# Kernel tuning notes

Hardware: AMD Instinct MI355X
Metric: run time of the kernel (lower is better)

The kernel has to match this reference:

```python
import jax, jax.numpy as jnp
import numpy as np

D_MODEL = 1024
N_HEADS = 16
D_FF = 512  # FeedForward default d_ff=512 (not overridden in EncoderLayer)
EPS = 1e-6


def _norm(x, alpha, bias):
    # Custom NormLayer: mean + UNBIASED variance (torch.var default, N-1 denom)
    mean = jnp.mean(x, axis=-1, keepdims=True)
    n = x.shape[-1]
    var = jnp.sum((x - mean) ** 2, axis=-1, keepdims=True) / (n - 1)
    return alpha * (x - mean) / jnp.sqrt(var + EPS) + bias


def setup_inputs() -> dict:
    key = jax.random.key(0)
    ks = jax.random.split(key, 12)
    s = 1.0 / np.sqrt(D_MODEL)
    inp = {
        "x": jax.random.normal(ks[0], (2, 2048, D_MODEL), dtype=jnp.float32),
        "Wq": jax.random.uniform(ks[1], (D_MODEL, D_MODEL), jnp.float32, -s, s),
        "bq": jnp.zeros((D_MODEL,), jnp.float32),
        "Wk": jax.random.uniform(ks[2], (D_MODEL, D_MODEL), jnp.float32, -s, s),
        "bk": jnp.zeros((D_MODEL,), jnp.float32),
        "Wv": jax.random.uniform(ks[3], (D_MODEL, D_MODEL), jnp.float32, -s, s),
        "bv": jnp.zeros((D_MODEL,), jnp.float32),
        "Wo": jax.random.uniform(ks[4], (D_MODEL, D_MODEL), jnp.float32, -s, s),
        "bo": jnp.zeros((D_MODEL,), jnp.float32),
        "alpha1": jnp.ones((D_MODEL,), jnp.float32),
        "beta1": jnp.zeros((D_MODEL,), jnp.float32),
        "alpha2": jnp.ones((D_MODEL,), jnp.float32),
        "beta2": jnp.zeros((D_MODEL,), jnp.float32),
        "W1": jax.random.uniform(ks[5], (D_MODEL, D_FF), jnp.float32, -s, s),
        "b1": jnp.zeros((D_FF,), jnp.float32),
        "W2": jax.random.uniform(ks[6], (D_FF, D_MODEL), jnp.float32, -1.0 / np.sqrt(D_FF), 1.0 / np.sqrt(D_FF)),
        "b2": jnp.zeros((D_MODEL,), jnp.float32),
    }
    return inp


def reference(x, Wq, bq, Wk, bk, Wv, bv, Wo, bo, alpha1, beta1, alpha2, beta2, W1, b1, W2, b2):
    B, S, D = x.shape
    H = N_HEADS
    dh = D // H
    # norm_1 applied to x, result feeds BOTH attention and the residual
    x = _norm(x, alpha1, beta1)
    # multihead attention (dropout = identity in eval)
    q = (x @ Wq + bq).reshape(B, S, H, dh)
    k = (x @ Wk + bk).reshape(B, S, H, dh)
    v = (x @ Wv + bv).reshape(B, S, H, dh)
    scores = jnp.einsum("bqhd,bkhd->bhqk", q, k) / jnp.sqrt(jnp.asarray(dh, x.dtype))
    attn = jax.nn.softmax(scores, axis=-1)
    o = jnp.einsum("bhqk,bkhd->bqhd", attn, v).reshape(B, S, D)
    o = o @ Wo + bo
    x = x + o
    # FFN on norm_2(x)
    h = _norm(x, alpha2, beta2)
    h = jax.nn.relu(h @ W1 + b1) @ W2 + b2
    return x + h
```

## Files before the change

kernel.cpp:

```cpp
#include <hip/hip_runtime.h>

typedef __bf16 bf16;
typedef __bf16 bf16x4 __attribute__((ext_vector_type(4)));
typedef __bf16 bf16x8 __attribute__((ext_vector_type(8)));
typedef float f32x4 __attribute__((ext_vector_type(4)));

#define D_MODEL 1024
#define SEQ 2048
#define NB 2
#define LOG2E 1.4426950408889634f

__device__ __forceinline__ void glds16(const bf16* g, bf16* l) {
    __builtin_amdgcn_global_load_lds(
        (const __attribute__((address_space(1))) void*)g,
        (__attribute__((address_space(3))) void*)l, 16, 0, 0);
}

__device__ __forceinline__ void tile_tcvt(
    const float* __restrict__ src, int rows, int cols, bf16* __restrict__ dst,
    int bx, int by, bf16 (*t)[72])
{
    int tid = threadIdx.x;
    int k0 = by * 64, n0 = bx * 64;
    int r = tid >> 2, c = (tid & 3) * 16;
    const float4* s = (const float4*)(src + (size_t)(k0 + r) * cols + n0 + c);
#pragma unroll
    for (int q = 0; q < 4; ++q) {
        float4 v = s[q];
        t[c + q * 4 + 0][r] = (bf16)v.x;
        t[c + q * 4 + 1][r] = (bf16)v.y;
        t[c + q * 4 + 2][r] = (bf16)v.z;
        t[c + q * 4 + 3][r] = (bf16)v.w;
    }
    __syncthreads();
    bf16* d = dst + (size_t)(n0 + r) * rows + k0 + c;
    *(bf16x8*)(d)     = *(const bf16x8*)&t[r][c];
    *(bf16x8*)(d + 8) = *(const bf16x8*)&t[r][c + 8];
}

__global__ __launch_bounds__(256) void prep_kernel(
    const float* __restrict__ Wq, const float* __restrict__ Wk,
    const float* __restrict__ Wv, const float* __restrict__ Wo,
    const float* __restrict__ W1, const float* __restrict__ W2,
    const float* __restrict__ bq, const float* __restrict__ bk,
    const float* __restrict__ bv,
    bf16* __restrict__ Wqkv_t, bf16* __restrict__ Wo_t,
    bf16* __restrict__ W1_t, bf16* __restrict__ W2_t,
    float* __restrict__ b_qkv)
{
    __shared__ bf16 t[64][72];
    int id = blockIdx.x;
    if (id < 1024) {
        int which = id >> 8, tile = id & 255;
        const float* src = which == 0 ? Wq : which == 1 ? Wk : which == 2 ? Wv : Wo;
        bf16* dst = which == 3 ? Wo_t : Wqkv_t + (size_t)which * 1024 * 1024;
        tile_tcvt(src, 1024, 1024, dst, tile & 15, tile >> 4, t);
    } else if (id < 1152) {
        int tile = id - 1024;
        tile_tcvt(W1, 1024, 512, W1_t, tile & 7, tile >> 3, t);
    } else if (id < 1280) {
        int tile = id - 1152;
        tile_tcvt(W2, 512, 1024, W2_t, tile & 15, tile >> 4, t);
    } else {
        int i = (id - 1280) * 256 + threadIdx.x;
        float v;
        if (i < 1024) v = bq[i];
        else if (i < 2048) v = bk[i - 1024];
        else v = bv[i - 2048];
        b_qkv[i] = v;
    }
}

__global__ __launch_bounds__(256) void norm_kernel(
    const float* __restrict__ X, const float* __restrict__ alpha,
    const float* __restrict__ beta, bf16* __restrict__ Y)
{
    int row = blockIdx.x;
    int tid = threadIdx.x;
    float4 v = ((const float4*)(X + (size_t)row * D_MODEL))[tid];
    float s = v.x + v.y + v.z + v.w;
    float ss = v.x*v.x + v.y*v.y + v.z*v.z + v.w*v.w;
#pragma unroll
    for (int off = 1; off < 64; off <<= 1) {
        s  += __shfl_xor(s, off, 64);
        ss += __shfl_xor(ss, off, 64);
    }
    __shared__ float sd[8];
    int wave = tid >> 6, lane = tid & 63;
    if (lane == 0) { sd[wave] = s; sd[4 + wave] = ss; }
    __syncthreads();
    s  = sd[0] + sd[1] + sd[2] + sd[3];
    ss = sd[4] + sd[5] + sd[6] + sd[7];
    float mean = s * (1.0f / 1024.0f);
    float var  = (ss - s * mean) * (1.0f / 1023.0f);
    float rs = rsqrtf(var + 1e-6f);
    float4 a = ((const float4*)alpha)[tid];
    float4 bt = ((const float4*)beta)[tid];
    bf16x4 o;
    o[0] = (bf16)(a.x * (v.x - mean) * rs + bt.x);
    o[1] = (bf16)(a.y * (v.y - mean) * rs + bt.y);
    o[2] = (bf16)(a.z * (v.z - mean) * rs + bt.z);
    o[3] = (bf16)(a.w * (v.w - mean) * rs + bt.w);
    *(bf16x4*)(Y + (size_t)row * D_MODEL + tid * 4) = o;
}

template <typename OutT, int BN, bool VFUSE>
__global__ __launch_bounds__(256) void gemm128(
    const bf16* __restrict__ A, const bf16* __restrict__ Bt,
    const float* __restrict__ bias, const bf16* __restrict__ Rb,
    const float* __restrict__ Rf, OutT* __restrict__ C, bf16* __restrict__ vT,
    int M, int N, int K, int lda, int relu)
{
    constexpr int NT = BN / 32;
    __shared__ bf16 As[128 * 32];
    __shared__ bf16 Bs[BN * 32];

    int tid = threadIdx.x;
    int wave = tid >> 6, lane = tid & 63;
    int quad = lane >> 4, l16 = lane & 15;
    int m0 = blockIdx.y * 128, n0 = blockIdx.x * BN;
    int wm = (wave >> 1) * 64, wn = (wave & 1) * (BN / 2);

    f32x4 acc[4][NT] = {};

    const bf16* ga = A  + (size_t)(m0 + (tid >> 2)) * lda + (tid & 3) * 8;
    const bf16* gb = Bt + (size_t)(n0 + (tid >> 2)) * K   + (tid & 3) * 8;
    bf16* lAs = As + wave * 512;
    bf16* lBs = Bs + wave * 512;

    for (int k0 = 0; k0 < K; k0 += 32) {
        __syncthreads();
        glds16(ga + k0, lAs);
        glds16(ga + (size_t)64 * lda + k0, lAs + 2048);
        glds16(gb + k0, lBs);
        if (BN == 128) glds16(gb + (size_t)64 * K + k0, lBs + 2048);
        __syncthreads();
        bf16x8 af[4], bfr[NT];
#pragma unroll
        for (int mt = 0; mt < 4; ++mt)
            af[mt] = *(const bf16x8*)(As + (wm + mt * 16 + l16) * 32 + quad * 8);
#pragma unroll
        for (int nt = 0; nt < NT; ++nt)
            bfr[nt] = *(const bf16x8*)(Bs + (wn + nt * 16 + l16) * 32 + quad * 8);
#pragma unroll
        for (int mt = 0; mt < 4; ++mt)
#pragma unroll
            for (int nt = 0; nt < NT; ++nt)
                acc[mt][nt] = __builtin_amdgcn_mfma_f32_16x16x32_bf16(af[mt], bfr[nt], acc[mt][nt], 0, 0, 0);
    }

#pragma unroll
    for (int nt = 0; nt < NT; ++nt) {
        int n = n0 + wn + nt * 16 + l16;
        float bv = bias[n];
        if (VFUSE && n >= 2048) {
            int d = n & 63, h = (n - 2048) >> 6;
#pragma unroll
            for (int mt = 0; mt < 4; ++mt) {
                int m = m0 + wm + mt * 16 + quad * 4;
                int b = m >> 11, sidx = m & 2047;
                bf16x4 pk;
#pragma unroll
                for (int r = 0; r < 4; ++r) pk[r] = (bf16)(acc[mt][nt][r] + bv);
                *(bf16x4*)(vT + (((size_t)(b * 16 + h) * 64 + d) * SEQ + sidx)) = pk;
            }
        } else {
#pragma unroll
            for (int mt = 0; mt < 4; ++mt) {
#pragma unroll
                for (int r = 0; r < 4; ++r) {
                    int m = m0 + wm + mt * 16 + quad * 4 + r;
                    float vv = acc[mt][nt][r] + bv;
                    if (Rb) vv += (float)Rb[(size_t)m * N + n];
                    if (Rf) vv += Rf[(size_t)m * N + n];
                    if (relu) vv = vv > 0.0f ? vv : 0.0f;
                    C[(size_t)m * N + n] = (OutT)vv;
                }
            }
        }
    }
}

__global__ __launch_bounds__(256) void attn_kernel(
    const bf16* __restrict__ qkv, const bf16* __restrict__ vT, bf16* __restrict__ O)
{
    __shared__ bf16 Ks[64][72];
    __shared__ bf16 Vt[64][72];
    __shared__ bf16 Ps[4][32][72];

    int tid = threadIdx.x;
    int wave = tid >> 6, lane = tid & 63;
    int quad = lane >> 4, l16 = lane & 15;
    int bh = blockIdx.y, b = bh >> 4, h = bh & 15;
    int q0 = blockIdx.x * 128;

    const bf16* Qb = qkv + (size_t)(b * SEQ + q0 + wave * 32) * 3072 + h * 64;
    const bf16* Kb = qkv + (size_t)(b * SEQ) * 3072 + 1024 + h * 64;
    const bf16* Vb = vT + (size_t)bh * 64 * SEQ;

    const float c_l2 = 0.125f * LOG2E;
    bf16x8 qa[2][2];
#pragma unroll
    for (int mt = 0; mt < 2; ++mt)
#pragma unroll
        for (int hf = 0; hf < 2; ++hf) {
            bf16x8 raw = *(const bf16x8*)(Qb + (size_t)(mt * 16 + l16) * 3072 + hf * 32 + quad * 8);
            bf16x8 sc;
#pragma unroll
            for (int j = 0; j < 8; ++j) sc[j] = (bf16)((float)raw[j] * c_l2);
            qa[mt][hf] = sc;
        }

    float lsum[2][4] = {};
    f32x4 oacc[2][4] = {};

    int sr = tid >> 2, scol = (tid & 3) * 16;
    const bf16* kp = Kb + (size_t)sr * 3072 + scol;
    const bf16* vp = Vb + (size_t)sr * SEQ + scol;

    bf16x8 kr0 = ((const bf16x8*)kp)[0];
    bf16x8 kr1 = ((const bf16x8*)kp)[1];
    bf16x8 vr0 = ((const bf16x8*)vp)[0];
    bf16x8 vr1 = ((const bf16x8*)vp)[1];

    for (int kt = 0; kt < SEQ; kt += 64) {
        __syncthreads();
        *(bf16x8*)&Ks[sr][scol]     = kr0;
        *(bf16x8*)&Ks[sr][scol + 8] = kr1;
        *(bf16x8*)&Vt[sr][scol]     = vr0;
        *(bf16x8*)&Vt[sr][scol + 8] = vr1;
        __syncthreads();

        if (kt + 64 < SEQ) {
            const bf16* kn = kp + (size_t)(kt + 64) * 3072;
            const bf16* vn = vp + kt + 64;
            kr0 = ((const bf16x8*)kn)[0];
            kr1 = ((const bf16x8*)kn)[1];
            vr0 = ((const bf16x8*)vn)[0];
            vr1 = ((const bf16x8*)vn)[1];
        }

        bf16x8 kb[4][2];
#pragma unroll
        for (int t4 = 0; t4 < 4; ++t4) {
            kb[t4][0] = *(const bf16x8*)&Ks[t4 * 16 + l16][quad * 8];
            kb[t4][1] = *(const bf16x8*)&Ks[t4 * 16 + l16][32 + quad * 8];
        }
        bf16x8 vb[4][2];
#pragma unroll
        for (int dt = 0; dt < 4; ++dt) {
            vb[dt][0] = *(const bf16x8*)&Vt[dt * 16 + l16][quad * 8];
            vb[dt][1] = *(const bf16x8*)&Vt[dt * 16 + l16][32 + quad * 8];
        }
#pragma unroll
        for (int mt = 0; mt < 2; ++mt)
#pragma unroll
            for (int t4 = 0; t4 < 4; ++t4) {
                f32x4 c = {};
                c = __builtin_amdgcn_mfma_f32_16x16x32_bf16(qa[mt][0], kb[t4][0], c, 0, 0, 0);
                c = __builtin_amdgcn_mfma_f32_16x16x32_bf16(qa[mt][1], kb[t4][1], c, 0, 0, 0);
#pragma unroll
                for (int r = 0; r < 4; ++r) {
                    float p = exp2f(c[r]);
                    lsum[mt][r] += p;
                    Ps[wave][mt * 16 + quad * 4 + r][t4 * 16 + l16] = (bf16)p;
                }
            }
#pragma unroll
        for (int mt = 0; mt < 2; ++mt) {
            bf16x8 pa0 = *(const bf16x8*)&Ps[wave][mt * 16 + l16][quad * 8];
            bf16x8 pa1 = *(const bf16x8*)&Ps[wave][mt * 16 + l16][32 + quad * 8];
#pragma unroll
            for (int dt = 0; dt < 4; ++dt) {
                oacc[mt][dt] = __builtin_amdgcn_mfma_f32_16x16x32_bf16(pa0, vb[dt][0], oacc[mt][dt], 0, 0, 0);
                oacc[mt][dt] = __builtin_amdgcn_mfma_f32_16x16x32_bf16(pa1, vb[dt][1], oacc[mt][dt], 0, 0, 0);
            }
        }
    }
#pragma unroll
    for (int mt = 0; mt < 2; ++mt)
#pragma unroll
        for (int r = 0; r < 4; ++r) {
            float l = lsum[mt][r];
            l += __shfl_xor(l, 1);
            l += __shfl_xor(l, 2);
            l += __shfl_xor(l, 4);
            l += __shfl_xor(l, 8);
            float inv = 1.0f / l;
            int row = b * SEQ + q0 + wave * 32 + mt * 16 + quad * 4 + r;
            bf16* op = O + (size_t)row * D_MODEL + h * 64;
#pragma unroll
            for (int dt = 0; dt < 4; ++dt)
                op[dt * 16 + l16] = (bf16)(oacc[mt][dt][r] * inv);
        }
}

extern "C" void kernel_launch(void* const* d_in, const int* in_sizes, int n_in,
                              void* d_out, int out_size, void* d_ws, size_t ws_size,
                              hipStream_t stream)
{
    const float* x      = (const float*)d_in[0];
    const float* Wq     = (const float*)d_in[1];
    const float* bq     = (const float*)d_in[2];
    const float* Wk     = (const float*)d_in[3];
    const float* bk     = (const float*)d_in[4];
    const float* Wv     = (const float*)d_in[5];
    const float* bv     = (const float*)d_in[6];
    const float* Wo     = (const float*)d_in[7];
    const float* bo     = (const float*)d_in[8];
    const float* alpha1 = (const float*)d_in[9];
    const float* beta1  = (const float*)d_in[10];
    const float* alpha2 = (const float*)d_in[11];
    const float* beta2  = (const float*)d_in[12];
    const float* W1     = (const float*)d_in[13];
    const float* b1     = (const float*)d_in[14];
    const float* W2     = (const float*)d_in[15];
    const float* b2     = (const float*)d_in[16];

    char* ws = (char*)d_ws;
    const size_t MB = 1ull << 20;
    bf16*  Wqkv_t = (bf16*)(ws + 0 * MB);
    bf16*  Wo_t   = (bf16*)(ws + 6 * MB);
    bf16*  W1_t   = (bf16*)(ws + 8 * MB);
    bf16*  W2_t   = (bf16*)(ws + 9 * MB);
    float* b_qkv  = (float*)(ws + 10 * MB);
    bf16*  xn     = (bf16*)(ws + 11 * MB);
    bf16*  qkv    = (bf16*)(ws + 19 * MB);
    bf16*  vT     = (bf16*)(ws + 43 * MB);
    bf16*  o      = (bf16*)(ws + 51 * MB);
    float* x2     = (float*)(ws + 19 * MB);
    bf16*  hn     = (bf16*)(ws + 35 * MB);
    bf16*  h1     = (bf16*)(ws + 43 * MB);

    const int M = NB * SEQ;

    prep_kernel<<<1292, 256, 0, stream>>>(Wq, Wk, Wv, Wo, W1, W2, bq, bk, bv,
                                          Wqkv_t, Wo_t, W1_t, W2_t, b_qkv);

    norm_kernel<<<M, 256, 0, stream>>>(x, alpha1, beta1, xn);

    gemm128<bf16, 128, true><<<dim3(24, 32), 256, 0, stream>>>(
        xn, Wqkv_t, b_qkv, nullptr, nullptr, qkv, vT, M, 3072, D_MODEL, D_MODEL, 0);

    attn_kernel<<<dim3(SEQ / 128, 32), 256, 0, stream>>>(qkv, vT, o);

    gemm128<float, 128, false><<<dim3(8, 32), 256, 0, stream>>>(
        o, Wo_t, bo, xn, nullptr, x2, nullptr, M, D_MODEL, D_MODEL, D_MODEL, 0);

    norm_kernel<<<M, 256, 0, stream>>>(x2, alpha2, beta2, hn);

    gemm128<bf16, 64, false><<<dim3(8, 32), 256, 0, stream>>>(
        hn, W1_t, b1, nullptr, nullptr, h1, nullptr, M, 512, D_MODEL, D_MODEL, 1);

    gemm128<float, 128, false><<<dim3(8, 32), 256, 0, stream>>>(
        h1, W2_t, b2, nullptr, x2, (float*)d_out, nullptr, M, D_MODEL, 512, 512, 0);
}
```

Measured before the change: 317.5 us.

## Split-K the Wo and W1 GEMMs with fused combine kernels; transpose attention scores

The Wo and FF1 GEMMs now split K across two blocks in z and write fp32 partials. The partials are then summed in new combine kernels that also fold in the bias and residual plus norm_2 (cnorm), or the bias plus ReLU (crelu). The QKV GEMM double-unrolls K per barrier, and the final GEMM uses BN=64 to launch more blocks. In attention, the QK^T MFMA operands are swapped so each lane writes a packed bf16x4 row of P and the row-sum reduction needs fewer shuffles. This trades extra fp32 partial traffic and workspace reuse for more blocks in flight on the 256-CU device and fewer LDS stores in attention.

```diff
diff --git a/kernel.cpp b/kernel.cpp
--- a/kernel.cpp
+++ b/kernel.cpp
@@ -104,49 +104,136 @@
     *(bf16x4*)(Y + (size_t)row * D_MODEL + tid * 4) = o;
 }
 
-template <typename OutT, int BN, bool VFUSE>
+__global__ __launch_bounds__(256) void cnorm_kernel(
+    const float* __restrict__ p0, const float* __restrict__ p1,
+    const bf16* __restrict__ xn, const float* __restrict__ bo,
+    const float* __restrict__ alpha, const float* __restrict__ beta,
+    float* __restrict__ x2, bf16* __restrict__ hn)
+{
+    int row = blockIdx.x;
+    int tid = threadIdx.x;
+    float4 a = ((const float4*)(p0 + (size_t)row * D_MODEL))[tid];
+    float4 b = ((const float4*)(p1 + (size_t)row * D_MODEL))[tid];
+    float4 bb = ((const float4*)bo)[tid];
+    bf16x4 xv = *(const bf16x4*)(xn + (size_t)row * D_MODEL + tid * 4);
+    float4 v;
+    v.x = a.x + b.x + bb.x + (float)xv[0];
+    v.y = a.y + b.y + bb.y + (float)xv[1];
+    v.z = a.z + b.z + bb.z + (float)xv[2];
+    v.w = a.w + b.w + bb.w + (float)xv[3];
+    ((float4*)(x2 + (size_t)row * D_MODEL))[tid] = v;
+    float s = v.x + v.y + v.z + v.w;
+    float ss = v.x*v.x + v.y*v.y + v.z*v.z + v.w*v.w;
+#pragma unroll
+    for (int off = 1; off < 64; off <<= 1) {
+        s  += __shfl_xor(s, off, 64);
+        ss += __shfl_xor(ss, off, 64);
+    }
+    __shared__ float sd[8];
+    int wave = tid >> 6, lane = tid & 63;
+    if (lane == 0) { sd[wave] = s; sd[4 + wave] = ss; }
+    __syncthreads();
+    s  = sd[0] + sd[1] + sd[2] + sd[3];
+    ss = sd[4] + sd[5] + sd[6] + sd[7];
+    float mean = s * (1.0f / 1024.0f);
+    float var  = (ss - s * mean) * (1.0f / 1023.0f);
+    float rs = rsqrtf(var + 1e-6f);
+    float4 al = ((const float4*)alpha)[tid];
+    float4 bt = ((const float4*)beta)[tid];
+    bf16x4 o;
+    o[0] = (bf16)(al.x * (v.x - mean) * rs + bt.x);
+    o[1] = (bf16)(al.y * (v.y - mean) * rs + bt.y);
+    o[2] = (bf16)(al.z * (v.z - mean) * rs + bt.z);
+    o[3] = (bf16)(al.w * (v.w - mean) * rs + bt.w);
+    *(bf16x4*)(hn + (size_t)row * D_MODEL + tid * 4) = o;
+}
+
+__global__ __launch_bounds__(256) void crelu_kernel(
+    const float* __restrict__ p0, const float* __restrict__ p1,
+    const float* __restrict__ b1, bf16* __restrict__ h1)
+{
+    int i = blockIdx.x * 256 + threadIdx.x;
+    float4 a = ((const float4*)p0)[i];
+    float4 b = ((const float4*)p1)[i];
+    int col = (i * 4) & 511;
+    float4 bb = *(const float4*)(b1 + col);
+    bf16x4 o;
+    o[0] = (bf16)fmaxf(a.x + b.x + bb.x, 0.0f);
+    o[1] = (bf16)fmaxf(a.y + b.y + bb.y, 0.0f);
+    o[2] = (bf16)fmaxf(a.z + b.z + bb.z, 0.0f);
+    o[3] = (bf16)fmaxf(a.w + b.w + bb.w, 0.0f);
+    ((bf16x4*)h1)[i] = o;
+}
+
+template <typename OutT, int BN, int KU, bool VFUSE, bool SPLITK>
 __global__ __launch_bounds__(256) void gemm128(
     const bf16* __restrict__ A, const bf16* __restrict__ Bt,
-    const float* __restrict__ bias, const bf16* __restrict__ Rb,
-    const float* __restrict__ Rf, OutT* __restrict__ C, bf16* __restrict__ vT,
+    const float* __restrict__ bias, const float* __restrict__ Rf,
+    OutT* __restrict__ C, bf16* __restrict__ vT,
     int M, int N, int K, int lda, int relu)
 {
     constexpr int NT = BN / 32;
-    __shared__ bf16 As[128 * 32];
-    __shared__ bf16 Bs[BN * 32];
+    constexpr int ASTR = 128 * 32;
+    constexpr int BSTR = BN * 32;
+    __shared__ bf16 As[ASTR * KU];
+    __shared__ bf16 Bs[BSTR * KU];
 
     int tid = threadIdx.x;
     int wave = tid >> 6, lane = tid & 63;
     int quad = lane >> 4, l16 = lane & 15;
     int m0 = blockIdx.y * 128, n0 = blockIdx.x * BN;
     int wm = (wave >> 1) * 64, wn = (wave & 1) * (BN / 2);
+    int Keff = SPLITK ? (K >> 1) : K;
+    int klo  = SPLITK ? blockIdx.z * Keff : 0;
 
     f32x4 acc[4][NT] = {};
 
-    const bf16* ga = A  + (size_t)(m0 + (tid >> 2)) * lda + (tid & 3) * 8;
-    const bf16* gb = Bt + (size_t)(n0 + (tid >> 2)) * K   + (tid & 3) * 8;
+    const bf16* ga = A  + (size_t)(m0 + (tid >> 2)) * lda + (tid & 3) * 8 + klo;
+    const bf16* gb = Bt + (size_t)(n0 + (tid >> 2)) * K   + (tid & 3) * 8 + klo;
     bf16* lAs = As + wave * 512;
     bf16* lBs = Bs + wave * 512;
 
-    for (int k0 = 0; k0 < K; k0 += 32) {
+    for (int k0 = 0; k0 < Keff; k0 += 32 * KU) {
         __syncthreads();
-        glds16(ga + k0, lAs);
-        glds16(ga + (size_t)64 * lda + k0, lAs + 2048);
-        glds16(gb + k0, lBs);
-        if (BN == 128) glds16(gb + (size_t)64 * K + k0, lBs + 2048);
+#pragma unroll
+        for (int u = 0; u < KU; ++u) {
+            glds16(ga + k0 + u * 32, lAs + u * ASTR);
+            glds16(ga + (size_t)64 * lda + k0 + u * 32, lAs + u * ASTR + 2048);
+            glds16(gb + k0 + u * 32, lBs + u * BSTR);
+            if (BN == 128) glds16(gb + (size_t)64 * K + k0 + u * 32, lBs + u * BSTR + 2048);
+        }
         __syncthreads();
-        bf16x8 af[4], bfr[NT];
-#pragma unroll
-        for (int mt = 0; mt < 4; ++mt)
-            af[mt] = *(const bf16x8*)(As + (wm + mt * 16 + l16) * 32 + quad * 8);
-#pragma unroll
-        for (int nt = 0; nt < NT; ++nt)
-            bfr[nt] = *(const bf16x8*)(Bs + (wn + nt * 16 + l16) * 32 + quad * 8);
-#pragma unroll
-        for (int mt = 0; mt < 4; ++mt)
+#pragma unroll
+        for (int u = 0; u < KU; ++u) {
+            bf16x8 af[4], bfr[NT];
+#pragma unroll
+            for (int mt = 0; mt < 4; ++mt)
+                af[mt] = *(const bf16x8*)(As + u * ASTR + (wm + mt * 16 + l16) * 32 + quad * 8);
 #pragma unroll
             for (int nt = 0; nt < NT; ++nt)
-                acc[mt][nt] = __builtin_amdgcn_mfma_f32_16x16x32_bf16(af[mt], bfr[nt], acc[mt][nt], 0, 0, 0);
+                bfr[nt] = *(const bf16x8*)(Bs + u * BSTR + (wn + nt * 16 + l16) * 32 + quad * 8);
+#pragma unroll
+            for (int mt = 0; mt < 4; ++mt)
+#pragma unroll
+                for (int nt = 0; nt < NT; ++nt)
+                    acc[mt][nt] = __builtin_amdgcn_mfma_f32_16x16x32_bf16(af[mt], bfr[nt], acc[mt][nt], 0, 0, 0);
+        }
+    }
+
+    if (SPLITK) {
+        float* P = (float*)C + (size_t)blockIdx.z * M * N;
+#pragma unroll
+        for (int nt = 0; nt < NT; ++nt) {
+            int n = n0 + wn + nt * 16 + l16;
+#pragma unroll
+            for (int mt = 0; mt < 4; ++mt)
+#pragma unroll
+                for (int r = 0; r < 4; ++r) {
+                    int m = m0 + wm + mt * 16 + quad * 4 + r;
+                    P[(size_t)m * N + n] = acc[mt][nt][r];
+                }
+        }
+        return;
     }
 
 #pragma unroll
@@ -171,7 +258,6 @@
                 for (int r = 0; r < 4; ++r) {
                     int m = m0 + wm + mt * 16 + quad * 4 + r;
                     float vv = acc[mt][nt][r] + bv;
-                    if (Rb) vv += (float)Rb[(size_t)m * N + n];
                     if (Rf) vv += Rf[(size_t)m * N + n];
                     if (relu) vv = vv > 0.0f ? vv : 0.0f;
                     C[(size_t)m * N + n] = (OutT)vv;
@@ -211,7 +297,7 @@
             qa[mt][hf] = sc;
         }
 
-    float lsum[2][4] = {};
+    float lsum[2] = {};
     f32x4 oacc[2][4] = {};
 
     int sr = tid >> 2, scol = (tid & 3) * 16;
@@ -257,14 +343,18 @@
 #pragma unroll
             for (int t4 = 0; t4 < 4; ++t4) {
                 f32x4 c = {};
-                c = __builtin_amdgcn_mfma_f32_16x16x32_bf16(qa[mt][0], kb[t4][0], c, 0, 0, 0);
-                c = __builtin_amdgcn_mfma_f32_16x16x32_bf16(qa[mt][1], kb[t4][1], c, 0, 0, 0);
+                c = __builtin_amdgcn_mfma_f32_16x16x32_bf16(kb[t4][0], qa[mt][0], c, 0, 0, 0);
+                c = __builtin_amdgcn_mfma_f32_16x16x32_bf16(kb[t4][1], qa[mt][1], c, 0, 0, 0);
+                bf16x4 pk;
+                float psum = 0.0f;
 #pragma unroll
                 for (int r = 0; r < 4; ++r) {
                     float p = exp2f(c[r]);
-                    lsum[mt][r] += p;
-                    Ps[wave][mt * 16 + quad * 4 + r][t4 * 16 + l16] = (bf16)p;
+                    psum += p;
+                    pk[r] = (bf16)p;
                 }
+                lsum[mt] += psum;
+                *(bf16x4*)&Ps[wave][mt * 16 + l16][t4 * 16 + quad * 4] = pk;
             }
 #pragma unroll
         for (int mt = 0; mt < 2; ++mt) {
@@ -278,21 +368,20 @@
         }
     }
 #pragma unroll
-    for (int mt = 0; mt < 2; ++mt)
+    for (int mt = 0; mt < 2; ++mt) {
+        float lr = lsum[mt];
+        lr += __shfl_xor(lr, 16);
+        lr += __shfl_xor(lr, 32);
 #pragma unroll
         for (int r = 0; r < 4; ++r) {
-            float l = lsum[mt][r];
-            l += __shfl_xor(l, 1);
-            l += __shfl_xor(l, 2);
-            l += __shfl_xor(l, 4);
-            l += __shfl_xor(l, 8);
-            float inv = 1.0f / l;
+            float inv = 1.0f / __shfl(lr, quad * 4 + r, 16);
             int row = b * SEQ + q0 + wave * 32 + mt * 16 + quad * 4 + r;
             bf16* op = O + (size_t)row * D_MODEL + h * 64;
 #pragma unroll
             for (int dt = 0; dt < 4; ++dt)
                 op[dt * 16 + l16] = (bf16)(oacc[mt][dt][r] * inv);
         }
+    }
 }
 
 extern "C" void kernel_launch(void* const* d_in, const int* in_sizes, int n_in,
@@ -328,9 +417,13 @@
     bf16*  qkv    = (bf16*)(ws + 19 * MB);
     bf16*  vT     = (bf16*)(ws + 43 * MB);
     bf16*  o      = (bf16*)(ws + 51 * MB);
+    float* pWo    = (float*)(ws + 19 * MB);
     float* x2     = (float*)(ws + 19 * MB);
-    bf16*  hn     = (bf16*)(ws + 35 * MB);
-    bf16*  h1     = (bf16*)(ws + 43 * MB);
+    bf16*  hn     = (bf16*)(ws + 51 * MB);
+    float* pF1    = (float*)(ws + 35 * MB);
+    bf16*  h1     = (bf16*)(ws + 35 * MB);
+    h1 = (bf16*)(ws + 55 * MB);
+    h1 = (bf16*)(ws + 11 * MB);
 
     const int M = NB * SEQ;
 
@@ -339,19 +432,23 @@
 
     norm_kernel<<<M, 256, 0, stream>>>(x, alpha1, beta1, xn);
 
-    gemm128<bf16, 128, true><<<dim3(24, 32), 256, 0, stream>>>(
-        xn, Wqkv_t, b_qkv, nullptr, nullptr, qkv, vT, M, 3072, D_MODEL, D_MODEL, 0);
+    gemm128<bf16, 128, 2, true, false><<<dim3(24, 32), 256, 0, stream>>>(
+        xn, Wqkv_t, b_qkv, nullptr, qkv, vT, M, 3072, D_MODEL, D_MODEL, 0);
 
     attn_kernel<<<dim3(SEQ / 128, 32), 256, 0, stream>>>(qkv, vT, o);
 
-    gemm128<float, 128, false><<<dim3(8, 32), 256, 0, stream>>>(
-        o, Wo_t, bo, xn, nullptr, x2, nullptr, M, D_MODEL, D_MODEL, D_MODEL, 0);
-
-    norm_kernel<<<M, 256, 0, stream>>>(x2, alpha2, beta2, hn);
-
-    gemm128<bf16, 64, false><<<dim3(8, 32), 256, 0, stream>>>(
-        hn, W1_t, b1, nullptr, nullptr, h1, nullptr, M, 512, D_MODEL, D_MODEL, 1);
-
-    gemm128<float, 128, false><<<dim3(8, 32), 256, 0, stream>>>(
-        h1, W2_t, b2, nullptr, x2, (float*)d_out, nullptr, M, D_MODEL, 512, 512, 0);
-}
+    gemm128<float, 128, 1, false, true><<<dim3(8, 32, 2), 256, 0, stream>>>(
+        o, Wo_t, nullptr, nullptr, pWo, nullptr, M, D_MODEL, D_MODEL, D_MODEL, 0);
+
+    cnorm_kernel<<<M, 256, 0, stream>>>(pWo, pWo + (size_t)M * D_MODEL, xn, bo,
+                                        alpha2, beta2, x2, hn);
+
+    gemm128<float, 64, 1, false, true><<<dim3(8, 32, 2), 256, 0, stream>>>(
+        hn, W1_t, nullptr, nullptr, pF1, nullptr, M, 512, D_MODEL, D_MODEL, 0);
+
+    crelu_kernel<<<(M * 512) / 1024, 256, 0, stream>>>(
+        pF1, pF1 + (size_t)M * 512, b1, h1);
+
+    gemm128<float, 64, 1, false, false><<<dim3(16, 32), 256, 0, stream>>>(
+        h1, W2_t, b2, x2, (float*)d_out, nullptr, M, D_MODEL, 512, 512, 0);
+}
```

New measurement: 283.2 us. 10.8% less time.
